# Optimization experiments

Hardware: AMD Instinct MI355X
Metric: run time of the kernel (lower is better)

The kernel has to match this reference:

```python
import jax, jax.numpy as jnp
import numpy as np

EMBED_DIM = 2048
NUM_HEADS = 16
HEAD_DIM = EMBED_DIM // NUM_HEADS  # 128
BLOCK_SIZE = 16
NUM_BLOCKS = 256  # max_seq_len 4096 / block_size 16
B = 64
T = 1  # single decode token per sequence (loop indexes k[i, 0, 0])


def setup_inputs() -> dict:
    key = jax.random.key(0)
    ks = jax.random.split(key, 12)
    w = 0.02
    return {
        "x": jax.random.normal(ks[0], (B, T, EMBED_DIM), jnp.float32),
        "k_cache": jax.random.normal(ks[1], (B, NUM_BLOCKS, BLOCK_SIZE, HEAD_DIM), jnp.float32),
        "v_cache": jax.random.normal(ks[2], (B, NUM_BLOCKS, BLOCK_SIZE, HEAD_DIM), jnp.float32),
        "cache_positions": jax.random.randint(ks[3], (B,), 0, NUM_BLOCKS * BLOCK_SIZE, jnp.int32),
        "Wq": jax.random.normal(ks[4], (EMBED_DIM, EMBED_DIM), jnp.float32) * w,
        "bq": jax.random.normal(ks[5], (EMBED_DIM,), jnp.float32) * w,
        "Wk": jax.random.normal(ks[6], (EMBED_DIM, HEAD_DIM), jnp.float32) * w,
        "bk": jax.random.normal(ks[7], (HEAD_DIM,), jnp.float32) * w,
        "Wv": jax.random.normal(ks[8], (EMBED_DIM, HEAD_DIM), jnp.float32) * w,
        "bv": jax.random.normal(ks[9], (HEAD_DIM,), jnp.float32) * w,
        "Wo": jax.random.normal(ks[10], (EMBED_DIM, EMBED_DIM), jnp.float32) * w,
        "bo": jax.random.normal(ks[11], (EMBED_DIM,), jnp.float32) * w,
    }


def reference(x, k_cache, v_cache, cache_positions, Wq, bq, Wk, bk, Wv, bv, Wo, bo):
    b, t, c = x.shape  # t == 1 (decode)
    hd = Wk.shape[1]
    h = c // hd
    scale = 1.0 / jnp.sqrt(jnp.asarray(hd, x.dtype))

    q = (x @ Wq + bq).reshape(b, t, h, hd)          # [B,1,H,hd]
    k_new = (x @ Wk + bk)[:, 0, :]                  # [B,hd] single KV head
    v_new = (x @ Wv + bv)[:, 0, :]                  # [B,hd]

    # Paged scatter: flatten (num_blocks, block_size) -> S slots; write new token at pos.
    s = k_cache.shape[1] * k_cache.shape[2]
    bidx = jnp.arange(b)
    kc = k_cache.reshape(b, s, hd).at[bidx, cache_positions].set(k_new)  # [B,S,hd]
    vc = v_cache.reshape(b, s, hd).at[bidx, cache_positions].set(v_new)

    # MQA: single KV head broadcast across H query heads. NOTE: softmax over the
    # FULL flattened cache (no validity mask), matching the original module.
    scores = jnp.einsum("bthd,bsd->bhts", q, kc) * scale   # [B,H,1,S]
    attn = jax.nn.softmax(scores, axis=-1)
    out = jnp.einsum("bhts,bsd->bthd", attn, vc).reshape(b, t, c)
    return out @ Wo + bo
```

## Files before the change

### kernel.cpp

```cpp
#include <hip/hip_runtime.h>
#include <math.h>

#define EMBED   2048
#define NHEADS  16
#define HD      128
#define S_TOT   4096
#define BATCH   64

typedef __attribute__((ext_vector_type(8))) short short8v;
typedef __attribute__((ext_vector_type(4))) short short4v;
typedef __attribute__((ext_vector_type(2))) short short2v;
typedef __attribute__((ext_vector_type(4))) float floatx4;

__device__ __forceinline__ unsigned short f2bf(float f) {
    unsigned u = __builtin_bit_cast(unsigned, f);
    u += 0x7fffu + ((u >> 16) & 1u);
    return (unsigned short)(u >> 16);
}

template <int CTRL>
__device__ __forceinline__ float dppf(float x) {
    int r = __builtin_amdgcn_mov_dpp(__builtin_bit_cast(int, x), CTRL, 0xF, 0xF, false);
    return __builtin_bit_cast(float, r);
}
__device__ __forceinline__ float rowmax16(float v) {
    v = fmaxf(v, dppf<0x121>(v));
    v = fmaxf(v, dppf<0x122>(v));
    v = fmaxf(v, dppf<0x124>(v));
    v = fmaxf(v, dppf<0x128>(v));
    return v;
}
__device__ __forceinline__ float rowsum16(float v) {
    v += dppf<0x121>(v);
    v += dppf<0x122>(v);
    v += dppf<0x124>(v);
    v += dppf<0x128>(v);
    return v;
}

__launch_bounds__(256)
__global__ void k1_qkv(const float* __restrict__ x,
                       const float* __restrict__ Wq, const float* __restrict__ bq,
                       const float* __restrict__ Wk, const float* __restrict__ bk,
                       const float* __restrict__ Wv, const float* __restrict__ bv,
                       float* __restrict__ qbuf, float* __restrict__ knew,
                       float* __restrict__ vnew) {
    const int tx = threadIdx.x & 31;
    const int ty = threadIdx.x >> 5;
    const int nt = blockIdx.x;
    const int kc = blockIdx.y;
    const int k0 = kc * 256;
    const int col0 = nt * 32;

    const float* W; const float* bias; float* out; int ldW;
    int cbase;
    if (col0 < 2048)       { W = Wq; bias = bq; out = qbuf; ldW = 2048; cbase = col0; }
    else if (col0 < 2176)  { W = Wk; bias = bk; out = knew; ldW = 128;  cbase = col0 - 2048; }
    else                   { W = Wv; bias = bv; out = vnew; ldW = 128;  cbase = col0 - 2176; }
    const int col = cbase + tx;

    __shared__ __align__(16) float xs[64][68];

    float acc[8] = {0, 0, 0, 0, 0, 0, 0, 0};

    for (int sub = 0; sub < 4; ++sub) {
        const int kb = k0 + sub * 64;
        #pragma unroll
        for (int i = 0; i < 4; ++i) {
            int c = threadIdx.x + i * 256;
            int r = c >> 4;
            int cc = (c & 15) << 2;
            float4 v = *(const float4*)(x + (size_t)r * EMBED + kb + cc);
            *(float4*)&xs[r][cc] = v;
        }
        __syncthreads();
        #pragma unroll
        for (int kk = 0; kk < 64; kk += 4) {
            float w0 = W[(size_t)(kb + kk + 0) * ldW + col];
            float w1 = W[(size_t)(kb + kk + 1) * ldW + col];
            float w2 = W[(size_t)(kb + kk + 2) * ldW + col];
            float w3 = W[(size_t)(kb + kk + 3) * ldW + col];
            #pragma unroll
            for (int j = 0; j < 8; ++j) {
                int m = ty + (j << 3);
                float4 xv = *(const float4*)&xs[m][kk];
                acc[j] = fmaf(xv.x, w0, acc[j]);
                acc[j] = fmaf(xv.y, w1, acc[j]);
                acc[j] = fmaf(xv.z, w2, acc[j]);
                acc[j] = fmaf(xv.w, w3, acc[j]);
            }
        }
        __syncthreads();
    }
    if (kc == 0) {
        float b = bias[col];
        #pragma unroll
        for (int j = 0; j < 8; ++j) acc[j] += b;
    }
    const int ldO = (ldW == 2048) ? 2048 : 128;
    #pragma unroll
    for (int j = 0; j < 8; ++j)
        atomicAdd(&out[(size_t)(ty + (j << 3)) * ldO + col], acc[j]);
}

__launch_bounds__(256)
__global__ void k2_attn(const float* __restrict__ qbuf,
                        const float* __restrict__ kcache,
                        const float* __restrict__ vcache,
                        const float* __restrict__ knew,
                        const float* __restrict__ vnew,
                        const int* __restrict__ cpos,
                        float* __restrict__ part_o,
                        float* __restrict__ part_ml)
{
    const int b = blockIdx.y;
    const int chunk = blockIdx.x;
    const int tid = threadIdx.x;
    const int w = tid >> 6;
    const int lane = tid & 63;
    const int quad = lane >> 4;
    const int lm = lane & 15;
    const int pos = cpos[b];

    __shared__ __align__(16) short qs[16 * 136];
    __shared__ __align__(16) short ksh[4][16 * 136];
    __shared__ __align__(16) short vsh[4][64 * 40];
    __shared__ __align__(16) short psh[4][16 * 40];

    {
        const int h = tid >> 4, d0 = (tid & 15) << 3;
        const float* src = qbuf + (size_t)b * EMBED + h * HD + d0;
        float4 a = *(const float4*)src;
        float4 c = *(const float4*)(src + 4);
        const float s = 0.08838834764831845f;
        short8v pk;
        pk[0] = f2bf(a.x * s); pk[1] = f2bf(a.y * s);
        pk[2] = f2bf(a.z * s); pk[3] = f2bf(a.w * s);
        pk[4] = f2bf(c.x * s); pk[5] = f2bf(c.y * s);
        pk[6] = f2bf(c.z * s); pk[7] = f2bf(c.w * s);
        *(short8v*)&qs[h * 136 + d0] = pk;
    }
    __syncthreads();

    short8v aq[4];
    #pragma unroll
    for (int t = 0; t < 4; ++t)
        aq[t] = *(short8v*)&qs[lm * 136 + t * 32 + quad * 8];

    short* kt = ksh[w];
    short* vt = vsh[w];
    short* pt = psh[w];

    float m_run[4] = {-INFINITY, -INFINITY, -INFINITY, -INFINITY};
    float l_run[4] = {0, 0, 0, 0};
    floatx4 oacc[8];
    #pragma unroll
    for (int i = 0; i < 8; ++i) oacc[i] = (floatx4){0, 0, 0, 0};

    const int sbase = chunk * 512 + w * 128;

    for (int st = 0; st < 4; ++st) {
        const int st0 = sbase + st * 32;
        floatx4 sc2[2];
        #pragma unroll
        for (int half = 0; half < 2; ++half) {
            const int s0 = st0 + half * 16;
            float4 tmp[8];
            #pragma unroll
            for (int i = 0; i < 8; ++i) {
                int f = i * 64 + lane;
                tmp[i] = *(const float4*)(kcache +
                    ((size_t)b * S_TOT + s0 + (f >> 5)) * HD + (f & 31) * 4);
            }
            #pragma unroll
            for (int i = 0; i < 8; ++i) {
                int f = i * 64 + lane;
                short4v pk;
                pk[0] = f2bf(tmp[i].x); pk[1] = f2bf(tmp[i].y);
                pk[2] = f2bf(tmp[i].z); pk[3] = f2bf(tmp[i].w);
                *(short4v*)&kt[(f >> 5) * 136 + (f & 31) * 4] = pk;
            }
            const int pr = pos - s0;
            if (pr >= 0 && pr < 16) {
                float2 kv = *(const float2*)(knew + b * HD + lane * 2);
                short2v p2; p2[0] = f2bf(kv.x); p2[1] = f2bf(kv.y);
                *(short2v*)&kt[pr * 136 + lane * 2] = p2;
            }
            floatx4 s = {0, 0, 0, 0};
            #pragma unroll
            for (int t = 0; t < 4; ++t) {
                short8v bk_ = *(short8v*)&kt[lm * 136 + t * 32 + quad * 8];
                s = __builtin_amdgcn_mfma_f32_16x16x32_bf16(aq[t], bk_, s, 0, 0, 0);
            }
            sc2[half] = s;
        }
        float alpha[4];
        #pragma unroll
        for (int r = 0; r < 4; ++r) {
            float mt = rowmax16(fmaxf(sc2[0][r], sc2[1][r]));
            float mn = fmaxf(m_run[r], mt);
            alpha[r] = __expf(m_run[r] - mn);
            m_run[r] = mn;
            float pA = __expf(sc2[0][r] - mn);
            float pB = __expf(sc2[1][r] - mn);
            float ss = rowsum16(pA + pB);
            l_run[r] = l_run[r] * alpha[r] + ss;
            pt[(quad * 4 + r) * 40 + lm]      = (short)f2bf(pA);
            pt[(quad * 4 + r) * 40 + 16 + lm] = (short)f2bf(pB);
        }
        #pragma unroll
        for (int dt = 0; dt < 8; ++dt) {
            oacc[dt][0] *= alpha[0]; oacc[dt][1] *= alpha[1];
            oacc[dt][2] *= alpha[2]; oacc[dt][3] *= alpha[3];
        }
        short8v ap = *(short8v*)&pt[lm * 40 + quad * 8];

        #pragma unroll
        for (int p = 0; p < 2; ++p) {
            const int sg = lane & 7;
            const int dgv = lane >> 3;
            #pragma unroll
            for (int i = 0; i < 2; ++i) {
                int dl = dgv * 4 + i * 32;
                int dglob = p * 64 + dl;
                const float* vb = vcache + ((size_t)b * S_TOT + st0 + sg * 4) * HD + dglob;
                float4 r0 = *(const float4*)(vb + 0 * HD);
                float4 r1 = *(const float4*)(vb + 1 * HD);
                float4 r2 = *(const float4*)(vb + 2 * HD);
                float4 r3 = *(const float4*)(vb + 3 * HD);
                short4v p0, p1, p2, p3;
                p0[0]=f2bf(r0.x); p0[1]=f2bf(r1.x); p0[2]=f2bf(r2.x); p0[3]=f2bf(r3.x);
                p1[0]=f2bf(r0.y); p1[1]=f2bf(r1.y); p1[2]=f2bf(r2.y); p1[3]=f2bf(r3.y);
                p2[0]=f2bf(r0.z); p2[1]=f2bf(r1.z); p2[2]=f2bf(r2.z); p2[3]=f2bf(r3.z);
                p3[0]=f2bf(r0.w); p3[1]=f2bf(r1.w); p3[2]=f2bf(r2.w); p3[3]=f2bf(r3.w);
                *(short4v*)&vt[(dl + 0) * 40 + sg * 4] = p0;
                *(short4v*)&vt[(dl + 1) * 40 + sg * 4] = p1;
                *(short4v*)&vt[(dl + 2) * 40 + sg * 4] = p2;
                *(short4v*)&vt[(dl + 3) * 40 + sg * 4] = p3;
            }
            const int prs = pos - st0;
            if (prs >= 0 && prs < 32) {
                float vvn = vnew[b * HD + p * 64 + lane];
                vt[lane * 40 + prs] = (short)f2bf(vvn);
            }
            #pragma unroll
            for (int dq = 0; dq < 4; ++dq) {
                int dt = p * 4 + dq;
                short8v bv_ = *(short8v*)&vt[(dq * 16 + lm) * 40 + quad * 8];
                oacc[dt] = __builtin_amdgcn_mfma_f32_16x16x32_bf16(ap, bv_, oacc[dt], 0, 0, 0);
            }
        }
    }

    const int cw = chunk * 4 + w;
    float* po = part_o + (size_t)(b * 32 + cw) * 16 * 128;
    #pragma unroll
    for (int dt = 0; dt < 8; ++dt)
        #pragma unroll
        for (int r = 0; r < 4; ++r)
            po[(quad * 4 + r) * 128 + dt * 16 + lm] = oacc[dt][r];
    if (lm < 2) {
        #pragma unroll
        for (int r = 0; r < 4; ++r) {
            float v = (lm == 0) ? m_run[r] : l_run[r];
            part_ml[((size_t)(b * 32 + cw) * 16 + quad * 4 + r) * 2 + lm] = v;
        }
    }
}

__launch_bounds__(128)
__global__ void k3_combine(const float* __restrict__ part_o,
                           const float* __restrict__ part_ml,
                           float* __restrict__ attn) {
    const int h = blockIdx.x, b = blockIdx.y, d = threadIdx.x;
    __shared__ float sm[32], sl[32];
    if (threadIdx.x < 32) {
        sm[threadIdx.x] = part_ml[((size_t)(b * 32 + threadIdx.x) * 16 + h) * 2 + 0];
        sl[threadIdx.x] = part_ml[((size_t)(b * 32 + threadIdx.x) * 16 + h) * 2 + 1];
    }
    __syncthreads();
    float M = -INFINITY;
    #pragma unroll
    for (int c = 0; c < 32; ++c) M = fmaxf(M, sm[c]);
    float O = 0.f, L = 0.f;
    for (int c = 0; c < 32; ++c) {
        float co = __expf(sm[c] - M);
        L += co * sl[c];
        O += co * part_o[((size_t)(b * 32 + c) * 16 + h) * 128 + d];
    }
    attn[(size_t)b * EMBED + h * HD + d] = O / L;
}

__launch_bounds__(256)
__global__ void k4_proj(const float* __restrict__ attn,
                        const float* __restrict__ Wo, const float* __restrict__ bo,
                        float* __restrict__ out) {
    const int tx = threadIdx.x & 31;
    const int ty = threadIdx.x >> 5;
    const int col = blockIdx.x * 32 + tx;
    const int k0 = blockIdx.y * 256;

    __shared__ __align__(16) float xs[64][68];
    float acc[8] = {0, 0, 0, 0, 0, 0, 0, 0};

    for (int sub = 0; sub < 4; ++sub) {
        const int kb = k0 + sub * 64;
        #pragma unroll
        for (int i = 0; i < 4; ++i) {
            int c = threadIdx.x + i * 256;
            int r = c >> 4;
            int cc = (c & 15) << 2;
            float4 v = *(const float4*)(attn + (size_t)r * EMBED + kb + cc);
            *(float4*)&xs[r][cc] = v;
        }
        __syncthreads();
        #pragma unroll
        for (int kk = 0; kk < 64; kk += 4) {
            float w0 = Wo[(size_t)(kb + kk + 0) * EMBED + col];
            float w1 = Wo[(size_t)(kb + kk + 1) * EMBED + col];
            float w2 = Wo[(size_t)(kb + kk + 2) * EMBED + col];
            float w3 = Wo[(size_t)(kb + kk + 3) * EMBED + col];
            #pragma unroll
            for (int j = 0; j < 8; ++j) {
                int m = ty + (j << 3);
                float4 xv = *(const float4*)&xs[m][kk];
                acc[j] = fmaf(xv.x, w0, acc[j]);
                acc[j] = fmaf(xv.y, w1, acc[j]);
                acc[j] = fmaf(xv.z, w2, acc[j]);
                acc[j] = fmaf(xv.w, w3, acc[j]);
            }
        }
        __syncthreads();
    }
    if (blockIdx.y == 0) {
        float b = bo[col];
        #pragma unroll
        for (int j = 0; j < 8; ++j) acc[j] += b;
    }
    #pragma unroll
    for (int j = 0; j < 8; ++j)
        atomicAdd(&out[(size_t)(ty + (j << 3)) * EMBED + col], acc[j]);
}

extern "C" void kernel_launch(void* const* d_in, const int* in_sizes, int n_in,
                              void* d_out, int out_size, void* d_ws, size_t ws_size,
                              hipStream_t stream) {
    (void)in_sizes; (void)n_in; (void)out_size; (void)ws_size;
    const float* x  = (const float*)d_in[0];
    const float* kc = (const float*)d_in[1];
    const float* vc = (const float*)d_in[2];
    const int*   cp = (const int*)d_in[3];
    const float* Wq = (const float*)d_in[4];
    const float* bq = (const float*)d_in[5];
    const float* Wk = (const float*)d_in[6];
    const float* bk = (const float*)d_in[7];
    const float* Wv = (const float*)d_in[8];
    const float* bv = (const float*)d_in[9];
    const float* Wo = (const float*)d_in[10];
    const float* bo = (const float*)d_in[11];
    float* out = (float*)d_out;
    float* ws  = (float*)d_ws;

    float* qbuf = ws;
    float* knew = ws + 131072;
    float* vnew = ws + 139264;
    float* attn = ws + 147456;
    float* po   = ws + 278528;
    float* pml  = ws + 4472832;

    hipMemsetAsync(qbuf, 0, 147456 * sizeof(float), stream);
    hipMemsetAsync(out, 0, (size_t)BATCH * EMBED * sizeof(float), stream);

    k1_qkv<<<dim3(72, 8), 256, 0, stream>>>(x, Wq, bq, Wk, bk, Wv, bv, qbuf, knew, vnew);
    k2_attn<<<dim3(8, 64), 256, 0, stream>>>(qbuf, kc, vc, knew, vnew, cp, po, pml);
    k3_combine<<<dim3(16, 64), 128, 0, stream>>>(po, pml, attn);
    k4_proj<<<dim3(64, 8), 256, 0, stream>>>(attn, Wo, bo, out);
}
```

Measured before the change: 394.8 us.

## Rebalance grids: wider GEMM tiles, finer split-K, attention chunks with in-block merge

```diff
diff --git a/kernel.cpp b/kernel.cpp
--- a/kernel.cpp
+++ b/kernel.cpp
@@ -47,63 +47,70 @@
                        float* __restrict__ vnew) {
     const int tx = threadIdx.x & 31;
     const int ty = threadIdx.x >> 5;
-    const int nt = blockIdx.x;
-    const int kc = blockIdx.y;
-    const int k0 = kc * 256;
-    const int col0 = nt * 32;
-
-    const float* W; const float* bias; float* out; int ldW;
-    int cbase;
+    const int col0 = blockIdx.x * 64;
+    const int kb = blockIdx.y * 64;
+
+    const float* W; const float* bias; float* out; int ldW; int cbase;
     if (col0 < 2048)       { W = Wq; bias = bq; out = qbuf; ldW = 2048; cbase = col0; }
     else if (col0 < 2176)  { W = Wk; bias = bk; out = knew; ldW = 128;  cbase = col0 - 2048; }
     else                   { W = Wv; bias = bv; out = vnew; ldW = 128;  cbase = col0 - 2176; }
-    const int col = cbase + tx;
+    const int c0 = cbase + tx;
+    const int c1 = cbase + 32 + tx;
 
     __shared__ __align__(16) float xs[64][68];
 
-    float acc[8] = {0, 0, 0, 0, 0, 0, 0, 0};
-
-    for (int sub = 0; sub < 4; ++sub) {
-        const int kb = k0 + sub * 64;
-        #pragma unroll
-        for (int i = 0; i < 4; ++i) {
-            int c = threadIdx.x + i * 256;
-            int r = c >> 4;
-            int cc = (c & 15) << 2;
-            float4 v = *(const float4*)(x + (size_t)r * EMBED + kb + cc);
-            *(float4*)&xs[r][cc] = v;
-        }
-        __syncthreads();
-        #pragma unroll
-        for (int kk = 0; kk < 64; kk += 4) {
-            float w0 = W[(size_t)(kb + kk + 0) * ldW + col];
-            float w1 = W[(size_t)(kb + kk + 1) * ldW + col];
-            float w2 = W[(size_t)(kb + kk + 2) * ldW + col];
-            float w3 = W[(size_t)(kb + kk + 3) * ldW + col];
-            #pragma unroll
-            for (int j = 0; j < 8; ++j) {
-                int m = ty + (j << 3);
-                float4 xv = *(const float4*)&xs[m][kk];
-                acc[j] = fmaf(xv.x, w0, acc[j]);
-                acc[j] = fmaf(xv.y, w1, acc[j]);
-                acc[j] = fmaf(xv.z, w2, acc[j]);
-                acc[j] = fmaf(xv.w, w3, acc[j]);
-            }
-        }
-        __syncthreads();
-    }
-    if (kc == 0) {
-        float b = bias[col];
-        #pragma unroll
-        for (int j = 0; j < 8; ++j) acc[j] += b;
-    }
-    const int ldO = (ldW == 2048) ? 2048 : 128;
-    #pragma unroll
-    for (int j = 0; j < 8; ++j)
-        atomicAdd(&out[(size_t)(ty + (j << 3)) * ldO + col], acc[j]);
-}
-
-__launch_bounds__(256)
+    #pragma unroll
+    for (int i = 0; i < 4; ++i) {
+        int c = threadIdx.x + i * 256;
+        int r = c >> 4;
+        int cc = (c & 15) << 2;
+        *(float4*)&xs[r][cc] = *(const float4*)(x + (size_t)r * EMBED + kb + cc);
+    }
+
+    float acc0[8] = {0, 0, 0, 0, 0, 0, 0, 0};
+    float acc1[8] = {0, 0, 0, 0, 0, 0, 0, 0};
+    __syncthreads();
+
+    #pragma unroll 4
+    for (int kk = 0; kk < 64; kk += 4) {
+        float w00 = W[(size_t)(kb + kk + 0) * ldW + c0];
+        float w01 = W[(size_t)(kb + kk + 1) * ldW + c0];
+        float w02 = W[(size_t)(kb + kk + 2) * ldW + c0];
+        float w03 = W[(size_t)(kb + kk + 3) * ldW + c0];
+        float w10 = W[(size_t)(kb + kk + 0) * ldW + c1];
+        float w11 = W[(size_t)(kb + kk + 1) * ldW + c1];
+        float w12 = W[(size_t)(kb + kk + 2) * ldW + c1];
+        float w13 = W[(size_t)(kb + kk + 3) * ldW + c1];
+        #pragma unroll
+        for (int j = 0; j < 8; ++j) {
+            float4 xv = *(const float4*)&xs[ty + (j << 3)][kk];
+            acc0[j] = fmaf(xv.x, w00, acc0[j]);
+            acc0[j] = fmaf(xv.y, w01, acc0[j]);
+            acc0[j] = fmaf(xv.z, w02, acc0[j]);
+            acc0[j] = fmaf(xv.w, w03, acc0[j]);
+            acc1[j] = fmaf(xv.x, w10, acc1[j]);
+            acc1[j] = fmaf(xv.y, w11, acc1[j]);
+            acc1[j] = fmaf(xv.z, w12, acc1[j]);
+            acc1[j] = fmaf(xv.w, w13, acc1[j]);
+        }
+    }
+    if (blockIdx.y == 0) {
+        float b0 = bias[c0], b1 = bias[c1];
+        #pragma unroll
+        for (int j = 0; j < 8; ++j) { acc0[j] += b0; acc1[j] += b1; }
+    }
+    #pragma unroll
+    for (int j = 0; j < 8; ++j) {
+        atomicAdd(&out[(size_t)(ty + (j << 3)) * ldW + c0], acc0[j]);
+        atomicAdd(&out[(size_t)(ty + (j << 3)) * ldW + c1], acc1[j]);
+    }
+}
+
+#define KT_SH (16 * 136)
+#define VT_SH (64 * 40)
+#define WAVE_SH (KT_SH + VT_SH)
+
+__launch_bounds__(256, 4)
 __global__ void k2_attn(const float* __restrict__ qbuf,
                         const float* __restrict__ kcache,
                         const float* __restrict__ vcache,
@@ -122,34 +129,27 @@
     const int lm = lane & 15;
     const int pos = cpos[b];
 
-    __shared__ __align__(16) short qs[16 * 136];
-    __shared__ __align__(16) short ksh[4][16 * 136];
-    __shared__ __align__(16) short vsh[4][64 * 40];
-    __shared__ __align__(16) short psh[4][16 * 40];
-
+    __shared__ __align__(16) short smem[4 * WAVE_SH];
+    short* kt = smem + w * WAVE_SH;
+    short* vt = kt + KT_SH;
+    short* pt = kt;
+
+    short8v aq[4];
     {
-        const int h = tid >> 4, d0 = (tid & 15) << 3;
-        const float* src = qbuf + (size_t)b * EMBED + h * HD + d0;
-        float4 a = *(const float4*)src;
-        float4 c = *(const float4*)(src + 4);
+        const float* qsrc = qbuf + (size_t)b * EMBED + lm * HD + quad * 8;
         const float s = 0.08838834764831845f;
-        short8v pk;
-        pk[0] = f2bf(a.x * s); pk[1] = f2bf(a.y * s);
-        pk[2] = f2bf(a.z * s); pk[3] = f2bf(a.w * s);
-        pk[4] = f2bf(c.x * s); pk[5] = f2bf(c.y * s);
-        pk[6] = f2bf(c.z * s); pk[7] = f2bf(c.w * s);
-        *(short8v*)&qs[h * 136 + d0] = pk;
-    }
-    __syncthreads();
-
-    short8v aq[4];
-    #pragma unroll
-    for (int t = 0; t < 4; ++t)
-        aq[t] = *(short8v*)&qs[lm * 136 + t * 32 + quad * 8];
-
-    short* kt = ksh[w];
-    short* vt = vsh[w];
-    short* pt = psh[w];
+        #pragma unroll
+        for (int t = 0; t < 4; ++t) {
+            float4 a = *(const float4*)(qsrc + t * 32);
+            float4 c = *(const float4*)(qsrc + t * 32 + 4);
+            short8v pk;
+            pk[0] = f2bf(a.x * s); pk[1] = f2bf(a.y * s);
+            pk[2] = f2bf(a.z * s); pk[3] = f2bf(a.w * s);
+            pk[4] = f2bf(c.x * s); pk[5] = f2bf(c.y * s);
+            pk[6] = f2bf(c.z * s); pk[7] = f2bf(c.w * s);
+            aq[t] = pk;
+        }
+    }
 
     float m_run[4] = {-INFINITY, -INFINITY, -INFINITY, -INFINITY};
     float l_run[4] = {0, 0, 0, 0};
@@ -157,9 +157,9 @@
     #pragma unroll
     for (int i = 0; i < 8; ++i) oacc[i] = (floatx4){0, 0, 0, 0};
 
-    const int sbase = chunk * 512 + w * 128;
-
-    for (int st = 0; st < 4; ++st) {
+    const int sbase = chunk * 256 + w * 64;
+
+    for (int st = 0; st < 2; ++st) {
         const int st0 = sbase + st * 32;
         floatx4 sc2[2];
         #pragma unroll
@@ -252,18 +252,54 @@
         }
     }
 
-    const int cw = chunk * 4 + w;
-    float* po = part_o + (size_t)(b * 32 + cw) * 16 * 128;
-    #pragma unroll
-    for (int dt = 0; dt < 8; ++dt)
-        #pragma unroll
-        for (int r = 0; r < 4; ++r)
-            po[(quad * 4 + r) * 128 + dt * 16 + lm] = oacc[dt][r];
-    if (lm < 2) {
+    __syncthreads();
+    float* pool = (float*)smem;
+    const int hr = quad * 4;
+    if (w & 1) {
+        float* dst = pool + (w >> 1) * 2080;
+        if (lm == 0) {
+            #pragma unroll
+            for (int r = 0; r < 4; ++r) { dst[hr + r] = m_run[r]; dst[16 + hr + r] = l_run[r]; }
+        }
+        #pragma unroll
+        for (int dt = 0; dt < 8; ++dt)
+            #pragma unroll
+            for (int r = 0; r < 4; ++r)
+                dst[32 + (hr + r) * 128 + dt * 16 + lm] = oacc[dt][r];
+    }
+    __syncthreads();
+    if ((w & 1) == 0) {
+        float* src = pool + (w >> 1) * 2080;
+        float a1[4], a2[4];
         #pragma unroll
         for (int r = 0; r < 4; ++r) {
-            float v = (lm == 0) ? m_run[r] : l_run[r];
-            part_ml[((size_t)(b * 32 + cw) * 16 + quad * 4 + r) * 2 + lm] = v;
+            float m2 = src[hr + r], l2 = src[16 + hr + r];
+            float M = fmaxf(m_run[r], m2);
+            a1[r] = __expf(m_run[r] - M);
+            a2[r] = __expf(m2 - M);
+            l_run[r] = l_run[r] * a1[r] + l2 * a2[r];
+            m_run[r] = M;
+        }
+        #pragma unroll
+        for (int dt = 0; dt < 8; ++dt)
+            #pragma unroll
+            for (int r = 0; r < 4; ++r)
+                oacc[dt][r] = oacc[dt][r] * a1[r] +
+                              src[32 + (hr + r) * 128 + dt * 16 + lm] * a2[r];
+
+        const int cw = chunk * 2 + (w >> 1);
+        float* po = part_o + (size_t)(b * 32 + cw) * 16 * 128;
+        #pragma unroll
+        for (int dt = 0; dt < 8; ++dt)
+            #pragma unroll
+            for (int r = 0; r < 4; ++r)
+                po[(hr + r) * 128 + dt * 16 + lm] = oacc[dt][r];
+        if (lm < 2) {
+            #pragma unroll
+            for (int r = 0; r < 4; ++r) {
+                float v = (lm == 0) ? m_run[r] : l_run[r];
+                part_ml[((size_t)(b * 32 + cw) * 16 + hr + r) * 2 + lm] = v;
+            }
         }
     }
 }
@@ -282,13 +318,23 @@
     float M = -INFINITY;
     #pragma unroll
     for (int c = 0; c < 32; ++c) M = fmaxf(M, sm[c]);
-    float O = 0.f, L = 0.f;
+    float co[32];
+    float L = 0.f;
+    #pragma unroll
     for (int c = 0; c < 32; ++c) {
-        float co = __expf(sm[c] - M);
-        L += co * sl[c];
-        O += co * part_o[((size_t)(b * 32 + c) * 16 + h) * 128 + d];
-    }
-    attn[(size_t)b * EMBED + h * HD + d] = O / L;
+        co[c] = __expf(sm[c] - M);
+        L += co[c] * sl[c];
+    }
+    const float* base = part_o + ((size_t)(b * 32) * 16 + h) * 128 + d;
+    float O0 = 0.f, O1 = 0.f, O2 = 0.f, O3 = 0.f;
+    #pragma unroll
+    for (int c = 0; c < 32; c += 4) {
+        O0 += co[c + 0] * base[(size_t)(c + 0) * 2048];
+        O1 += co[c + 1] * base[(size_t)(c + 1) * 2048];
+        O2 += co[c + 2] * base[(size_t)(c + 2) * 2048];
+        O3 += co[c + 3] * base[(size_t)(c + 3) * 2048];
+    }
+    attn[(size_t)b * EMBED + h * HD + d] = (O0 + O1 + O2 + O3) / L;
 }
 
 __launch_bounds__(256)
@@ -297,49 +343,56 @@
                         float* __restrict__ out) {
     const int tx = threadIdx.x & 31;
     const int ty = threadIdx.x >> 5;
-    const int col = blockIdx.x * 32 + tx;
-    const int k0 = blockIdx.y * 256;
+    const int c0 = blockIdx.x * 64 + tx;
+    const int c1 = blockIdx.x * 64 + 32 + tx;
+    const int kb = blockIdx.y * 64;
 
     __shared__ __align__(16) float xs[64][68];
-    float acc[8] = {0, 0, 0, 0, 0, 0, 0, 0};
-
-    for (int sub = 0; sub < 4; ++sub) {
-        const int kb = k0 + sub * 64;
-        #pragma unroll
-        for (int i = 0; i < 4; ++i) {
-            int c = threadIdx.x + i * 256;
-            int r = c >> 4;
-            int cc = (c & 15) << 2;
-            float4 v = *(const float4*)(attn + (size_t)r * EMBED + kb + cc);
-            *(float4*)&xs[r][cc] = v;
-        }
-        __syncthreads();
-        #pragma unroll
-        for (int kk = 0; kk < 64; kk += 4) {
-            float w0 = Wo[(size_t)(kb + kk + 0) * EMBED + col];
-            float w1 = Wo[(size_t)(kb + kk + 1) * EMBED + col];
-            float w2 = Wo[(size_t)(kb + kk + 2) * EMBED + col];
-            float w3 = Wo[(size_t)(kb + kk + 3) * EMBED + col];
-            #pragma unroll
-            for (int j = 0; j < 8; ++j) {
-                int m = ty + (j << 3);
-                float4 xv = *(const float4*)&xs[m][kk];
-                acc[j] = fmaf(xv.x, w0, acc[j]);
-                acc[j] = fmaf(xv.y, w1, acc[j]);
-                acc[j] = fmaf(xv.z, w2, acc[j]);
-                acc[j] = fmaf(xv.w, w3, acc[j]);
-            }
-        }
-        __syncthreads();
+    #pragma unroll
+    for (int i = 0; i < 4; ++i) {
+        int c = threadIdx.x + i * 256;
+        int r = c >> 4;
+        int cc = (c & 15) << 2;
+        *(float4*)&xs[r][cc] = *(const float4*)(attn + (size_t)r * EMBED + kb + cc);
+    }
+
+    float acc0[8] = {0, 0, 0, 0, 0, 0, 0, 0};
+    float acc1[8] = {0, 0, 0, 0, 0, 0, 0, 0};
+    __syncthreads();
+
+    #pragma unroll 4
+    for (int kk = 0; kk < 64; kk += 4) {
+        float w00 = Wo[(size_t)(kb + kk + 0) * EMBED + c0];
+        float w01 = Wo[(size_t)(kb + kk + 1) * EMBED + c0];
+        float w02 = Wo[(size_t)(kb + kk + 2) * EMBED + c0];
+        float w03 = Wo[(size_t)(kb + kk + 3) * EMBED + c0];
+        float w10 = Wo[(size_t)(kb + kk + 0) * EMBED + c1];
+        float w11 = Wo[(size_t)(kb + kk + 1) * EMBED + c1];
+        float w12 = Wo[(size_t)(kb + kk + 2) * EMBED + c1];
+        float w13 = Wo[(size_t)(kb + kk + 3) * EMBED + c1];
+        #pragma unroll
+        for (int j = 0; j < 8; ++j) {
+            float4 xv = *(const float4*)&xs[ty + (j << 3)][kk];
+            acc0[j] = fmaf(xv.x, w00, acc0[j]);
+            acc0[j] = fmaf(xv.y, w01, acc0[j]);
+            acc0[j] = fmaf(xv.z, w02, acc0[j]);
+            acc0[j] = fmaf(xv.w, w03, acc0[j]);
+            acc1[j] = fmaf(xv.x, w10, acc1[j]);
+            acc1[j] = fmaf(xv.y, w11, acc1[j]);
+            acc1[j] = fmaf(xv.z, w12, acc1[j]);
+            acc1[j] = fmaf(xv.w, w13, acc1[j]);
+        }
     }
     if (blockIdx.y == 0) {
-        float b = bo[col];
-        #pragma unroll
-        for (int j = 0; j < 8; ++j) acc[j] += b;
-    }
-    #pragma unroll
-    for (int j = 0; j < 8; ++j)
-        atomicAdd(&out[(size_t)(ty + (j << 3)) * EMBED + col], acc[j]);
+        float b0 = bo[c0], b1 = bo[c1];
+        #pragma unroll
+        for (int j = 0; j < 8; ++j) { acc0[j] += b0; acc1[j] += b1; }
+    }
+    #pragma unroll
+    for (int j = 0; j < 8; ++j) {
+        atomicAdd(&out[(size_t)(ty + (j << 3)) * EMBED + c0], acc0[j]);
+        atomicAdd(&out[(size_t)(ty + (j << 3)) * EMBED + c1], acc1[j]);
+    }
 }
 
 extern "C" void kernel_launch(void* const* d_in, const int* in_sizes, int n_in,
@@ -371,8 +424,8 @@
     hipMemsetAsync(qbuf, 0, 147456 * sizeof(float), stream);
     hipMemsetAsync(out, 0, (size_t)BATCH * EMBED * sizeof(float), stream);
 
-    k1_qkv<<<dim3(72, 8), 256, 0, stream>>>(x, Wq, bq, Wk, bk, Wv, bv, qbuf, knew, vnew);
-    k2_attn<<<dim3(8, 64), 256, 0, stream>>>(qbuf, kc, vc, knew, vnew, cp, po, pml);
+    k1_qkv<<<dim3(36, 32), 256, 0, stream>>>(x, Wq, bq, Wk, bk, Wv, bv, qbuf, knew, vnew);
+    k2_attn<<<dim3(16, 64), 256, 0, stream>>>(qbuf, kc, vc, knew, vnew, cp, po, pml);
     k3_combine<<<dim3(16, 64), 128, 0, stream>>>(po, pml, attn);
-    k4_proj<<<dim3(64, 8), 256, 0, stream>>>(attn, Wo, bo, out);
-}
+    k4_proj<<<dim3(32, 32), 256, 0, stream>>>(attn, Wo, bo, out);
+}
```

Result: slower. 421.8 us (+6.8%).

## Replace atomic split-K GEMMs with partial buffers and register-direct attention operands

Applied to the files above, without the earlier changes.

```diff
diff --git a/kernel.cpp b/kernel.cpp
--- a/kernel.cpp
+++ b/kernel.cpp
@@ -9,7 +9,6 @@
 
 typedef __attribute__((ext_vector_type(8))) short short8v;
 typedef __attribute__((ext_vector_type(4))) short short4v;
-typedef __attribute__((ext_vector_type(2))) short short2v;
 typedef __attribute__((ext_vector_type(4))) float floatx4;
 
 __device__ __forceinline__ unsigned short f2bf(float f) {
@@ -18,89 +17,98 @@
     return (unsigned short)(u >> 16);
 }
 
-template <int CTRL>
-__device__ __forceinline__ float dppf(float x) {
-    int r = __builtin_amdgcn_mov_dpp(__builtin_bit_cast(int, x), CTRL, 0xF, 0xF, false);
-    return __builtin_bit_cast(float, r);
-}
-__device__ __forceinline__ float rowmax16(float v) {
-    v = fmaxf(v, dppf<0x121>(v));
-    v = fmaxf(v, dppf<0x122>(v));
-    v = fmaxf(v, dppf<0x124>(v));
-    v = fmaxf(v, dppf<0x128>(v));
-    return v;
-}
-__device__ __forceinline__ float rowsum16(float v) {
-    v += dppf<0x121>(v);
-    v += dppf<0x122>(v);
-    v += dppf<0x124>(v);
-    v += dppf<0x128>(v);
-    return v;
-}
-
 __launch_bounds__(256)
 __global__ void k1_qkv(const float* __restrict__ x,
-                       const float* __restrict__ Wq, const float* __restrict__ bq,
-                       const float* __restrict__ Wk, const float* __restrict__ bk,
-                       const float* __restrict__ Wv, const float* __restrict__ bv,
-                       float* __restrict__ qbuf, float* __restrict__ knew,
-                       float* __restrict__ vnew) {
+                       const float* __restrict__ Wq, const float* __restrict__ Wk,
+                       const float* __restrict__ Wv, float* __restrict__ kp) {
     const int tx = threadIdx.x & 31;
     const int ty = threadIdx.x >> 5;
-    const int nt = blockIdx.x;
-    const int kc = blockIdx.y;
-    const int k0 = kc * 256;
-    const int col0 = nt * 32;
-
-    const float* W; const float* bias; float* out; int ldW;
-    int cbase;
-    if (col0 < 2048)       { W = Wq; bias = bq; out = qbuf; ldW = 2048; cbase = col0; }
-    else if (col0 < 2176)  { W = Wk; bias = bk; out = knew; ldW = 128;  cbase = col0 - 2048; }
-    else                   { W = Wv; bias = bv; out = vnew; ldW = 128;  cbase = col0 - 2176; }
-    const int col = cbase + tx;
-
-    __shared__ __align__(16) float xs[64][68];
-
-    float acc[8] = {0, 0, 0, 0, 0, 0, 0, 0};
-
-    for (int sub = 0; sub < 4; ++sub) {
-        const int kb = k0 + sub * 64;
-        #pragma unroll
-        for (int i = 0; i < 4; ++i) {
-            int c = threadIdx.x + i * 256;
-            int r = c >> 4;
-            int cc = (c & 15) << 2;
-            float4 v = *(const float4*)(x + (size_t)r * EMBED + kb + cc);
-            *(float4*)&xs[r][cc] = v;
-        }
-        __syncthreads();
-        #pragma unroll
-        for (int kk = 0; kk < 64; kk += 4) {
-            float w0 = W[(size_t)(kb + kk + 0) * ldW + col];
-            float w1 = W[(size_t)(kb + kk + 1) * ldW + col];
-            float w2 = W[(size_t)(kb + kk + 2) * ldW + col];
-            float w3 = W[(size_t)(kb + kk + 3) * ldW + col];
-            #pragma unroll
-            for (int j = 0; j < 8; ++j) {
-                int m = ty + (j << 3);
-                float4 xv = *(const float4*)&xs[m][kk];
-                acc[j] = fmaf(xv.x, w0, acc[j]);
-                acc[j] = fmaf(xv.y, w1, acc[j]);
-                acc[j] = fmaf(xv.z, w2, acc[j]);
-                acc[j] = fmaf(xv.w, w3, acc[j]);
-            }
-        }
-        __syncthreads();
-    }
-    if (kc == 0) {
-        float b = bias[col];
-        #pragma unroll
-        for (int j = 0; j < 8; ++j) acc[j] += b;
-    }
-    const int ldO = (ldW == 2048) ? 2048 : 128;
+    const int col0 = blockIdx.x * 128;
+    const int kb = blockIdx.y * 128;
+
+    const float* W; int ldW; int cbase;
+    if (col0 < 2048)       { W = Wq; ldW = 2048; cbase = col0; }
+    else if (col0 == 2048) { W = Wk; ldW = 128;  cbase = 0; }
+    else                   { W = Wv; ldW = 128;  cbase = 0; }
+    const int c4 = cbase + tx * 4;
+
+    __shared__ __align__(16) float xs[64][132];
+
+    #pragma unroll
+    for (int i = 0; i < 8; ++i) {
+        int c = threadIdx.x + i * 256;
+        int r = c >> 5;
+        int cc = (c & 31) << 2;
+        *(float4*)&xs[r][cc] = *(const float4*)(x + (size_t)r * EMBED + kb + cc);
+    }
+
+    float4 acc[8];
+    #pragma unroll
+    for (int j = 0; j < 8; ++j) acc[j] = make_float4(0.f, 0.f, 0.f, 0.f);
+    __syncthreads();
+
+    #pragma unroll 4
+    for (int kk = 0; kk < 128; kk += 4) {
+        const float* wr = W + (size_t)(kb + kk) * ldW + c4;
+        float4 wv0 = *(const float4*)(wr);
+        float4 wv1 = *(const float4*)(wr + ldW);
+        float4 wv2 = *(const float4*)(wr + 2 * (size_t)ldW);
+        float4 wv3 = *(const float4*)(wr + 3 * (size_t)ldW);
+        #pragma unroll
+        for (int j = 0; j < 8; ++j) {
+            float4 xv = *(const float4*)&xs[ty + (j << 3)][kk];
+            acc[j].x = fmaf(xv.x, wv0.x, acc[j].x);
+            acc[j].y = fmaf(xv.x, wv0.y, acc[j].y);
+            acc[j].z = fmaf(xv.x, wv0.z, acc[j].z);
+            acc[j].w = fmaf(xv.x, wv0.w, acc[j].w);
+            acc[j].x = fmaf(xv.y, wv1.x, acc[j].x);
+            acc[j].y = fmaf(xv.y, wv1.y, acc[j].y);
+            acc[j].z = fmaf(xv.y, wv1.z, acc[j].z);
+            acc[j].w = fmaf(xv.y, wv1.w, acc[j].w);
+            acc[j].x = fmaf(xv.z, wv2.x, acc[j].x);
+            acc[j].y = fmaf(xv.z, wv2.y, acc[j].y);
+            acc[j].z = fmaf(xv.z, wv2.z, acc[j].z);
+            acc[j].w = fmaf(xv.z, wv2.w, acc[j].w);
+            acc[j].x = fmaf(xv.w, wv3.x, acc[j].x);
+            acc[j].y = fmaf(xv.w, wv3.y, acc[j].y);
+            acc[j].z = fmaf(xv.w, wv3.z, acc[j].z);
+            acc[j].w = fmaf(xv.w, wv3.w, acc[j].w);
+        }
+    }
+    float* dst = kp + (size_t)blockIdx.y * 64 * 2304 + col0 + tx * 4;
     #pragma unroll
     for (int j = 0; j < 8; ++j)
-        atomicAdd(&out[(size_t)(ty + (j << 3)) * ldO + col], acc[j]);
+        *(float4*)&dst[(size_t)(ty + (j << 3)) * 2304] = acc[j];
+}
+
+__launch_bounds__(256)
+__global__ void k1b_reduce(const float* __restrict__ kp,
+                           const float* __restrict__ bq, const float* __restrict__ bk,
+                           const float* __restrict__ bv,
+                           float* __restrict__ qbuf, float* __restrict__ knew,
+                           float* __restrict__ vnew) {
+    const int idx = blockIdx.x * 256 + threadIdx.x;
+    const int r = idx / 576;
+    const int c4 = (idx - r * 576) * 4;
+    float4 s = make_float4(0.f, 0.f, 0.f, 0.f);
+    #pragma unroll
+    for (int sp = 0; sp < 16; ++sp) {
+        float4 v = *(const float4*)(kp + ((size_t)sp * 64 + r) * 2304 + c4);
+        s.x += v.x; s.y += v.y; s.z += v.z; s.w += v.w;
+    }
+    if (c4 < 2048) {
+        float4 b = *(const float4*)(bq + c4);
+        s.x += b.x; s.y += b.y; s.z += b.z; s.w += b.w;
+        *(float4*)&qbuf[(size_t)r * 2048 + c4] = s;
+    } else if (c4 < 2176) {
+        float4 b = *(const float4*)(bk + (c4 - 2048));
+        s.x += b.x; s.y += b.y; s.z += b.z; s.w += b.w;
+        *(float4*)&knew[(size_t)r * 128 + (c4 - 2048)] = s;
+    } else {
+        float4 b = *(const float4*)(bv + (c4 - 2176));
+        s.x += b.x; s.y += b.y; s.z += b.z; s.w += b.w;
+        *(float4*)&vnew[(size_t)r * 128 + (c4 - 2176)] = s;
+    }
 }
 
 __launch_bounds__(256)
@@ -122,149 +130,143 @@
     const int lm = lane & 15;
     const int pos = cpos[b];
 
-    __shared__ __align__(16) short qs[16 * 136];
-    __shared__ __align__(16) short ksh[4][16 * 136];
-    __shared__ __align__(16) short vsh[4][64 * 40];
-    __shared__ __align__(16) short psh[4][16 * 40];
-
+    __shared__ __align__(16) short pts[4][16][40];
+    short (*pt)[40] = pts[w];
+
+    const float scale = 0.08838834764831845f;
+    short8v bq_[4], knf[4];
     {
-        const int h = tid >> 4, d0 = (tid & 15) << 3;
-        const float* src = qbuf + (size_t)b * EMBED + h * HD + d0;
-        float4 a = *(const float4*)src;
-        float4 c = *(const float4*)(src + 4);
-        const float s = 0.08838834764831845f;
-        short8v pk;
-        pk[0] = f2bf(a.x * s); pk[1] = f2bf(a.y * s);
-        pk[2] = f2bf(a.z * s); pk[3] = f2bf(a.w * s);
-        pk[4] = f2bf(c.x * s); pk[5] = f2bf(c.y * s);
-        pk[6] = f2bf(c.z * s); pk[7] = f2bf(c.w * s);
-        *(short8v*)&qs[h * 136 + d0] = pk;
-    }
-    __syncthreads();
-
-    short8v aq[4];
-    #pragma unroll
-    for (int t = 0; t < 4; ++t)
-        aq[t] = *(short8v*)&qs[lm * 136 + t * 32 + quad * 8];
-
-    short* kt = ksh[w];
-    short* vt = vsh[w];
-    short* pt = psh[w];
-
-    float m_run[4] = {-INFINITY, -INFINITY, -INFINITY, -INFINITY};
-    float l_run[4] = {0, 0, 0, 0};
+        const float* qs = qbuf + (size_t)b * EMBED + lm * HD + quad * 8;
+        const float* ks = knew + b * HD + quad * 8;
+        #pragma unroll
+        for (int t = 0; t < 4; ++t) {
+            float4 a = *(const float4*)(qs + t * 32);
+            float4 c = *(const float4*)(qs + t * 32 + 4);
+            short8v pk;
+            pk[0] = f2bf(a.x * scale); pk[1] = f2bf(a.y * scale);
+            pk[2] = f2bf(a.z * scale); pk[3] = f2bf(a.w * scale);
+            pk[4] = f2bf(c.x * scale); pk[5] = f2bf(c.y * scale);
+            pk[6] = f2bf(c.z * scale); pk[7] = f2bf(c.w * scale);
+            bq_[t] = pk;
+            float4 ka = *(const float4*)(ks + t * 32);
+            float4 kc = *(const float4*)(ks + t * 32 + 4);
+            short8v pk2;
+            pk2[0] = f2bf(ka.x); pk2[1] = f2bf(ka.y);
+            pk2[2] = f2bf(ka.z); pk2[3] = f2bf(ka.w);
+            pk2[4] = f2bf(kc.x); pk2[5] = f2bf(kc.y);
+            pk2[6] = f2bf(kc.z); pk2[7] = f2bf(kc.w);
+            knf[t] = pk2;
+        }
+    }
+    unsigned short vnbf[8];
+    #pragma unroll
+    for (int dt = 0; dt < 8; ++dt)
+        vnbf[dt] = f2bf(vnew[b * HD + dt * 16 + lm]);
+
+    float m_run = -INFINITY, l_run = 0.f;
     floatx4 oacc[8];
     #pragma unroll
-    for (int i = 0; i < 8; ++i) oacc[i] = (floatx4){0, 0, 0, 0};
+    for (int i = 0; i < 8; ++i) oacc[i] = (floatx4){0.f, 0.f, 0.f, 0.f};
 
     const int sbase = chunk * 512 + w * 128;
 
+    #pragma unroll 2
     for (int st = 0; st < 4; ++st) {
         const int st0 = sbase + st * 32;
-        floatx4 sc2[2];
+        floatx4 sc[2];
         #pragma unroll
         for (int half = 0; half < 2; ++half) {
             const int s0 = st0 + half * 16;
-            float4 tmp[8];
+            const float* kr = kcache + ((size_t)b * S_TOT + s0 + lm) * HD + quad * 8;
+            short8v ak[4];
             #pragma unroll
-            for (int i = 0; i < 8; ++i) {
-                int f = i * 64 + lane;
-                tmp[i] = *(const float4*)(kcache +
-                    ((size_t)b * S_TOT + s0 + (f >> 5)) * HD + (f & 31) * 4);
-            }
-            #pragma unroll
-            for (int i = 0; i < 8; ++i) {
-                int f = i * 64 + lane;
-                short4v pk;
-                pk[0] = f2bf(tmp[i].x); pk[1] = f2bf(tmp[i].y);
-                pk[2] = f2bf(tmp[i].z); pk[3] = f2bf(tmp[i].w);
-                *(short4v*)&kt[(f >> 5) * 136 + (f & 31) * 4] = pk;
+            for (int t = 0; t < 4; ++t) {
+                float4 a = *(const float4*)(kr + t * 32);
+                float4 c = *(const float4*)(kr + t * 32 + 4);
+                short8v pk;
+                pk[0] = f2bf(a.x); pk[1] = f2bf(a.y);
+                pk[2] = f2bf(a.z); pk[3] = f2bf(a.w);
+                pk[4] = f2bf(c.x); pk[5] = f2bf(c.y);
+                pk[6] = f2bf(c.z); pk[7] = f2bf(c.w);
+                ak[t] = pk;
             }
             const int pr = pos - s0;
             if (pr >= 0 && pr < 16) {
-                float2 kv = *(const float2*)(knew + b * HD + lane * 2);
-                short2v p2; p2[0] = f2bf(kv.x); p2[1] = f2bf(kv.y);
-                *(short2v*)&kt[pr * 136 + lane * 2] = p2;
+                if (lm == pr) {
+                    ak[0] = knf[0]; ak[1] = knf[1];
+                    ak[2] = knf[2]; ak[3] = knf[3];
+                }
             }
-            floatx4 s = {0, 0, 0, 0};
+            floatx4 s = {0.f, 0.f, 0.f, 0.f};
             #pragma unroll
-            for (int t = 0; t < 4; ++t) {
-                short8v bk_ = *(short8v*)&kt[lm * 136 + t * 32 + quad * 8];
-                s = __builtin_amdgcn_mfma_f32_16x16x32_bf16(aq[t], bk_, s, 0, 0, 0);
+            for (int t = 0; t < 4; ++t)
+                s = __builtin_amdgcn_mfma_f32_16x16x32_bf16(ak[t], bq_[t], s, 0, 0, 0);
+            sc[half] = s;
+        }
+        float mt = fmaxf(fmaxf(fmaxf(sc[0][0], sc[0][1]), fmaxf(sc[0][2], sc[0][3])),
+                         fmaxf(fmaxf(sc[1][0], sc[1][1]), fmaxf(sc[1][2], sc[1][3])));
+        mt = fmaxf(mt, __shfl_xor(mt, 16));
+        mt = fmaxf(mt, __shfl_xor(mt, 32));
+        const float mn = fmaxf(m_run, mt);
+        const float alpha = __expf(m_run - mn);
+        m_run = mn;
+        const float p0 = __expf(sc[0][0] - mn), p1 = __expf(sc[0][1] - mn);
+        const float p2 = __expf(sc[0][2] - mn), p3 = __expf(sc[0][3] - mn);
+        const float p4 = __expf(sc[1][0] - mn), p5 = __expf(sc[1][1] - mn);
+        const float p6 = __expf(sc[1][2] - mn), p7 = __expf(sc[1][3] - mn);
+        float ss = ((p0 + p1) + (p2 + p3)) + ((p4 + p5) + (p6 + p7));
+        ss += __shfl_xor(ss, 16);
+        ss += __shfl_xor(ss, 32);
+        l_run = l_run * alpha + ss;
+        short4v w0, w1;
+        w0[0] = (short)f2bf(p0); w0[1] = (short)f2bf(p1);
+        w0[2] = (short)f2bf(p2); w0[3] = (short)f2bf(p3);
+        w1[0] = (short)f2bf(p4); w1[1] = (short)f2bf(p5);
+        w1[2] = (short)f2bf(p6); w1[3] = (short)f2bf(p7);
+        *(short4v*)&pt[lm][quad * 4]      = w0;
+        *(short4v*)&pt[lm][16 + quad * 4] = w1;
+        #pragma unroll
+        for (int dt = 0; dt < 8; ++dt) {
+            oacc[dt][0] *= alpha; oacc[dt][1] *= alpha;
+            oacc[dt][2] *= alpha; oacc[dt][3] *= alpha;
+        }
+        short8v ap = *(short8v*)&pt[lm][quad * 8];
+
+        const int prs = pos - st0;
+        const bool dosub = (prs >= 0 && prs < 32);
+        #pragma unroll
+        for (int dt = 0; dt < 8; ++dt) {
+            const float* vr = vcache + ((size_t)b * S_TOT + st0 + quad * 8) * HD + dt * 16 + lm;
+            float v0 = vr[0 * HD], v1 = vr[1 * HD], v2 = vr[2 * HD], v3 = vr[3 * HD];
+            float v4 = vr[4 * HD], v5 = vr[5 * HD], v6 = vr[6 * HD], v7 = vr[7 * HD];
+            short8v av;
+            av[0] = (short)f2bf(v0); av[1] = (short)f2bf(v1);
+            av[2] = (short)f2bf(v2); av[3] = (short)f2bf(v3);
+            av[4] = (short)f2bf(v4); av[5] = (short)f2bf(v5);
+            av[6] = (short)f2bf(v6); av[7] = (short)f2bf(v7);
+            if (dosub) {
+                const int jm = prs - quad * 8;
+                if (jm == 0) av[0] = (short)vnbf[dt];
+                if (jm == 1) av[1] = (short)vnbf[dt];
+                if (jm == 2) av[2] = (short)vnbf[dt];
+                if (jm == 3) av[3] = (short)vnbf[dt];
+                if (jm == 4) av[4] = (short)vnbf[dt];
+                if (jm == 5) av[5] = (short)vnbf[dt];
+                if (jm == 6) av[6] = (short)vnbf[dt];
+                if (jm == 7) av[7] = (short)vnbf[dt];
             }
-            sc2[half] = s;
-        }
-        float alpha[4];
-        #pragma unroll
-        for (int r = 0; r < 4; ++r) {
-            float mt = rowmax16(fmaxf(sc2[0][r], sc2[1][r]));
-            float mn = fmaxf(m_run[r], mt);
-            alpha[r] = __expf(m_run[r] - mn);
-            m_run[r] = mn;
-            float pA = __expf(sc2[0][r] - mn);
-            float pB = __expf(sc2[1][r] - mn);
-            float ss = rowsum16(pA + pB);
-            l_run[r] = l_run[r] * alpha[r] + ss;
-            pt[(quad * 4 + r) * 40 + lm]      = (short)f2bf(pA);
-            pt[(quad * 4 + r) * 40 + 16 + lm] = (short)f2bf(pB);
-        }
-        #pragma unroll
-        for (int dt = 0; dt < 8; ++dt) {
-            oacc[dt][0] *= alpha[0]; oacc[dt][1] *= alpha[1];
-            oacc[dt][2] *= alpha[2]; oacc[dt][3] *= alpha[3];
-        }
-        short8v ap = *(short8v*)&pt[lm * 40 + quad * 8];
-
-        #pragma unroll
-        for (int p = 0; p < 2; ++p) {
-            const int sg = lane & 7;
-            const int dgv = lane >> 3;
-            #pragma unroll
-            for (int i = 0; i < 2; ++i) {
-                int dl = dgv * 4 + i * 32;
-                int dglob = p * 64 + dl;
-                const float* vb = vcache + ((size_t)b * S_TOT + st0 + sg * 4) * HD + dglob;
-                float4 r0 = *(const float4*)(vb + 0 * HD);
-                float4 r1 = *(const float4*)(vb + 1 * HD);
-                float4 r2 = *(const float4*)(vb + 2 * HD);
-                float4 r3 = *(const float4*)(vb + 3 * HD);
-                short4v p0, p1, p2, p3;
-                p0[0]=f2bf(r0.x); p0[1]=f2bf(r1.x); p0[2]=f2bf(r2.x); p0[3]=f2bf(r3.x);
-                p1[0]=f2bf(r0.y); p1[1]=f2bf(r1.y); p1[2]=f2bf(r2.y); p1[3]=f2bf(r3.y);
-                p2[0]=f2bf(r0.z); p2[1]=f2bf(r1.z); p2[2]=f2bf(r2.z); p2[3]=f2bf(r3.z);
-                p3[0]=f2bf(r0.w); p3[1]=f2bf(r1.w); p3[2]=f2bf(r2.w); p3[3]=f2bf(r3.w);
-                *(short4v*)&vt[(dl + 0) * 40 + sg * 4] = p0;
-                *(short4v*)&vt[(dl + 1) * 40 + sg * 4] = p1;
-                *(short4v*)&vt[(dl + 2) * 40 + sg * 4] = p2;
-                *(short4v*)&vt[(dl + 3) * 40 + sg * 4] = p3;
-            }
-            const int prs = pos - st0;
-            if (prs >= 0 && prs < 32) {
-                float vvn = vnew[b * HD + p * 64 + lane];
-                vt[lane * 40 + prs] = (short)f2bf(vvn);
-            }
-            #pragma unroll
-            for (int dq = 0; dq < 4; ++dq) {
-                int dt = p * 4 + dq;
-                short8v bv_ = *(short8v*)&vt[(dq * 16 + lm) * 40 + quad * 8];
-                oacc[dt] = __builtin_amdgcn_mfma_f32_16x16x32_bf16(ap, bv_, oacc[dt], 0, 0, 0);
-            }
+            oacc[dt] = __builtin_amdgcn_mfma_f32_16x16x32_bf16(av, ap, oacc[dt], 0, 0, 0);
         }
     }
 
     const int cw = chunk * 4 + w;
-    float* po = part_o + (size_t)(b * 32 + cw) * 16 * 128;
+    float* po = part_o + (size_t)(b * 32 + cw) * (16 * 128);
     #pragma unroll
     for (int dt = 0; dt < 8; ++dt)
-        #pragma unroll
-        for (int r = 0; r < 4; ++r)
-            po[(quad * 4 + r) * 128 + dt * 16 + lm] = oacc[dt][r];
-    if (lm < 2) {
-        #pragma unroll
-        for (int r = 0; r < 4; ++r) {
-            float v = (lm == 0) ? m_run[r] : l_run[r];
-            part_ml[((size_t)(b * 32 + cw) * 16 + quad * 4 + r) * 2 + lm] = v;
-        }
+        *(floatx4*)&po[lm * 128 + dt * 16 + quad * 4] = oacc[dt];
+    if (quad == 0) {
+        float2 ml; ml.x = m_run; ml.y = l_run;
+        *(float2*)&part_ml[((size_t)(b * 32 + cw) * 16 + lm) * 2] = ml;
     }
 }
 
@@ -282,64 +284,97 @@
     float M = -INFINITY;
     #pragma unroll
     for (int c = 0; c < 32; ++c) M = fmaxf(M, sm[c]);
-    float O = 0.f, L = 0.f;
+    float co[32];
+    float L = 0.f;
+    #pragma unroll
     for (int c = 0; c < 32; ++c) {
-        float co = __expf(sm[c] - M);
-        L += co * sl[c];
-        O += co * part_o[((size_t)(b * 32 + c) * 16 + h) * 128 + d];
-    }
-    attn[(size_t)b * EMBED + h * HD + d] = O / L;
+        co[c] = __expf(sm[c] - M);
+        L += co[c] * sl[c];
+    }
+    const float* base = part_o + ((size_t)(b * 32) * 16 + h) * 128 + d;
+    float O0 = 0.f, O1 = 0.f, O2 = 0.f, O3 = 0.f;
+    #pragma unroll
+    for (int c = 0; c < 32; c += 4) {
+        O0 += co[c + 0] * base[(size_t)(c + 0) * 2048];
+        O1 += co[c + 1] * base[(size_t)(c + 1) * 2048];
+        O2 += co[c + 2] * base[(size_t)(c + 2) * 2048];
+        O3 += co[c + 3] * base[(size_t)(c + 3) * 2048];
+    }
+    attn[(size_t)b * EMBED + h * HD + d] = (O0 + O1 + O2 + O3) / L;
 }
 
 __launch_bounds__(256)
 __global__ void k4_proj(const float* __restrict__ attn,
-                        const float* __restrict__ Wo, const float* __restrict__ bo,
-                        float* __restrict__ out) {
+                        const float* __restrict__ Wo, float* __restrict__ k4p) {
     const int tx = threadIdx.x & 31;
     const int ty = threadIdx.x >> 5;
-    const int col = blockIdx.x * 32 + tx;
-    const int k0 = blockIdx.y * 256;
-
-    __shared__ __align__(16) float xs[64][68];
-    float acc[8] = {0, 0, 0, 0, 0, 0, 0, 0};
-
-    for (int sub = 0; sub < 4; ++sub) {
-        const int kb = k0 + sub * 64;
-        #pragma unroll
-        for (int i = 0; i < 4; ++i) {
-            int c = threadIdx.x + i * 256;
-            int r = c >> 4;
-            int cc = (c & 15) << 2;
-            float4 v = *(const float4*)(attn + (size_t)r * EMBED + kb + cc);
-            *(float4*)&xs[r][cc] = v;
-        }
-        __syncthreads();
-        #pragma unroll
-        for (int kk = 0; kk < 64; kk += 4) {
-            float w0 = Wo[(size_t)(kb + kk + 0) * EMBED + col];
-            float w1 = Wo[(size_t)(kb + kk + 1) * EMBED + col];
-            float w2 = Wo[(size_t)(kb + kk + 2) * EMBED + col];
-            float w3 = Wo[(size_t)(kb + kk + 3) * EMBED + col];
-            #pragma unroll
-            for (int j = 0; j < 8; ++j) {
-                int m = ty + (j << 3);
-                float4 xv = *(const float4*)&xs[m][kk];
-                acc[j] = fmaf(xv.x, w0, acc[j]);
-                acc[j] = fmaf(xv.y, w1, acc[j]);
-                acc[j] = fmaf(xv.z, w2, acc[j]);
-                acc[j] = fmaf(xv.w, w3, acc[j]);
-            }
-        }
-        __syncthreads();
-    }
-    if (blockIdx.y == 0) {
-        float b = bo[col];
-        #pragma unroll
-        for (int j = 0; j < 8; ++j) acc[j] += b;
-    }
+    const int col0 = blockIdx.x * 128;
+    const int kb = blockIdx.y * 128;
+    const int c4 = col0 + tx * 4;
+
+    __shared__ __align__(16) float xs[64][132];
+    #pragma unroll
+    for (int i = 0; i < 8; ++i) {
+        int c = threadIdx.x + i * 256;
+        int r = c >> 5;
+        int cc = (c & 31) << 2;
+        *(float4*)&xs[r][cc] = *(const float4*)(attn + (size_t)r * EMBED + kb + cc);
+    }
+
+    float4 acc[8];
+    #pragma unroll
+    for (int j = 0; j < 8; ++j) acc[j] = make_float4(0.f, 0.f, 0.f, 0.f);
+    __syncthreads();
+
+    #pragma unroll 4
+    for (int kk = 0; kk < 128; kk += 4) {
+        const float* wr = Wo + (size_t)(kb + kk) * EMBED + c4;
+        float4 wv0 = *(const float4*)(wr);
+        float4 wv1 = *(const float4*)(wr + EMBED);
+        float4 wv2 = *(const float4*)(wr + 2 * (size_t)EMBED);
+        float4 wv3 = *(const float4*)(wr + 3 * (size_t)EMBED);
+        #pragma unroll
+        for (int j = 0; j < 8; ++j) {
+            float4 xv = *(const float4*)&xs[ty + (j << 3)][kk];
+            acc[j].x = fmaf(xv.x, wv0.x, acc[j].x);
+            acc[j].y = fmaf(xv.x, wv0.y, acc[j].y);
+            acc[j].z = fmaf(xv.x, wv0.z, acc[j].z);
+            acc[j].w = fmaf(xv.x, wv0.w, acc[j].w);
+            acc[j].x = fmaf(xv.y, wv1.x, acc[j].x);
+            acc[j].y = fmaf(xv.y, wv1.y, acc[j].y);
+            acc[j].z = fmaf(xv.y, wv1.z, acc[j].z);
+            acc[j].w = fmaf(xv.y, wv1.w, acc[j].w);
+            acc[j].x = fmaf(xv.z, wv2.x, acc[j].x);
+            acc[j].y = fmaf(xv.z, wv2.y, acc[j].y);
+            acc[j].z = fmaf(xv.z, wv2.z, acc[j].z);
+            acc[j].w = fmaf(xv.z, wv2.w, acc[j].w);
+            acc[j].x = fmaf(xv.w, wv3.x, acc[j].x);
+            acc[j].y = fmaf(xv.w, wv3.y, acc[j].y);
+            acc[j].z = fmaf(xv.w, wv3.z, acc[j].z);
+            acc[j].w = fmaf(xv.w, wv3.w, acc[j].w);
+        }
+    }
+    float* dst = k4p + (size_t)blockIdx.y * 64 * 2048 + c4;
     #pragma unroll
     for (int j = 0; j < 8; ++j)
-        atomicAdd(&out[(size_t)(ty + (j << 3)) * EMBED + col], acc[j]);
+        *(float4*)&dst[(size_t)(ty + (j << 3)) * 2048] = acc[j];
+}
+
+__launch_bounds__(256)
+__global__ void k4b_reduce(const float* __restrict__ k4p,
+                           const float* __restrict__ bo, float* __restrict__ out) {
+    const int idx = blockIdx.x * 256 + threadIdx.x;
+    const int r = idx >> 9;
+    const int c4 = (idx & 511) * 4;
+    float4 s = make_float4(0.f, 0.f, 0.f, 0.f);
+    #pragma unroll
+    for (int sp = 0; sp < 16; ++sp) {
+        float4 v = *(const float4*)(k4p + ((size_t)sp * 64 + r) * 2048 + c4);
+        s.x += v.x; s.y += v.y; s.z += v.z; s.w += v.w;
+    }
+    float4 b = *(const float4*)(bo + c4);
+    s.x += b.x; s.y += b.y; s.z += b.z; s.w += b.w;
+    *(float4*)&out[(size_t)r * 2048 + c4] = s;
 }
 
 extern "C" void kernel_launch(void* const* d_in, const int* in_sizes, int n_in,
@@ -365,14 +400,13 @@
     float* knew = ws + 131072;
     float* vnew = ws + 139264;
     float* attn = ws + 147456;
-    float* po   = ws + 278528;
-    float* pml  = ws + 4472832;
-
-    hipMemsetAsync(qbuf, 0, 147456 * sizeof(float), stream);
-    hipMemsetAsync(out, 0, (size_t)BATCH * EMBED * sizeof(float), stream);
-
-    k1_qkv<<<dim3(72, 8), 256, 0, stream>>>(x, Wq, bq, Wk, bk, Wv, bv, qbuf, knew, vnew);
-    k2_attn<<<dim3(8, 64), 256, 0, stream>>>(qbuf, kc, vc, knew, vnew, cp, po, pml);
-    k3_combine<<<dim3(16, 64), 128, 0, stream>>>(po, pml, attn);
-    k4_proj<<<dim3(64, 8), 256, 0, stream>>>(attn, Wo, bo, out);
-}
+    float* pml  = ws + 278528;
+    float* big  = ws + 344064;
+
+    k1_qkv<<<dim3(18, 16), 256, 0, stream>>>(x, Wq, Wk, Wv, big);
+    k1b_reduce<<<dim3(144), 256, 0, stream>>>(big, bq, bk, bv, qbuf, knew, vnew);
+    k2_attn<<<dim3(8, 64), 256, 0, stream>>>(qbuf, kc, vc, knew, vnew, cp, big, pml);
+    k3_combine<<<dim3(16, 64), 128, 0, stream>>>(big, pml, attn);
+    k4_proj<<<dim3(16, 16), 256, 0, stream>>>(attn, Wo, big);
+    k4b_reduce<<<dim3(128), 256, 0, stream>>>(big, bo, out);
+}
```

Result: no change. 393.7 us (-0.3%).
